# Optimization experiments

Measured on AMD Instinct MI355X. Metric: run time of the kernel, lower is better.

Reference implementation:

```python
import jax, jax.numpy as jnp
import numpy as np
from jax import lax

M = 8   # num_heads
K = 4   # num_points


def conv2d(x, w, b, pad):
    # x: [B,C,H,W], w: [O,I,kh,kw]
    y = lax.conv_general_dilated(x, w, (1, 1), [(pad, pad), (pad, pad)],
                                 dimension_numbers=('NCHW', 'OIHW', 'NCHW'))
    return y + b[None, :, None, None]


def grid_sample_zeros(v, px, py):
    # Bilinear grid_sample, align_corners=True, padding_mode='zeros'.
    # v: [N,Cm,H,W]; px,py: [N,P] in pixel coordinates.
    N, Cm, H, W = v.shape
    x0 = jnp.floor(px); y0 = jnp.floor(py)
    x1 = x0 + 1.0;      y1 = y0 + 1.0
    wx = px - x0;       wy = py - y0
    vflat = v.reshape(N, Cm, H * W)

    def tap(xi, yi):
        valid = (xi >= 0) & (xi <= W - 1) & (yi >= 0) & (yi <= H - 1)
        xc = jnp.clip(xi, 0, W - 1).astype(jnp.int32)
        yc = jnp.clip(yi, 0, H - 1).astype(jnp.int32)
        idx = yc * W + xc                          # [N,P]
        g = jnp.take_along_axis(vflat, idx[:, None, :], axis=2)  # [N,Cm,P]
        return g * valid[:, None, :].astype(v.dtype)

    v00 = tap(x0, y0); v01 = tap(x1, y0)
    v10 = tap(x0, y1); v11 = tap(x1, y1)
    wx = wx[:, None, :]; wy = wy[:, None, :]
    return (v00 * (1 - wx) * (1 - wy) + v01 * wx * (1 - wy)
            + v10 * (1 - wx) * wy + v11 * wx * wy)


def setup_inputs() -> dict:
    key = jax.random.key(0)
    ks = jax.random.split(key, 16)
    B, C, H, W = 8, 256, 64, 64
    s = 0.02
    inp = {
        'f_recalib': jax.random.normal(ks[0], (B, C, H, W), jnp.float32),
        'f_orig':    jax.random.normal(ks[1], (B, C, H, W), jnp.float32),
        'offset_w': jax.random.normal(ks[2], (M * K * 2, C, 3, 3), jnp.float32) * s,
        'offset_b': jnp.zeros((M * K * 2,), jnp.float32),
        'attn_w':   jax.random.normal(ks[3], (M * K, C, 3, 3), jnp.float32) * s,
        'attn_b':   jnp.zeros((M * K,), jnp.float32),
        'value_w':  jax.random.normal(ks[4], (C, C, 1, 1), jnp.float32) * s,
        'value_b':  jnp.zeros((C,), jnp.float32),
        'proj_w':   jax.random.normal(ks[5], (C, C, 1, 1), jnp.float32) * s,
        'proj_b':   jnp.zeros((C,), jnp.float32),
        'mlp_w1':   jax.random.normal(ks[6], (2 * C, C, 1, 1), jnp.float32) * s,
        'mlp_b1':   jnp.zeros((2 * C,), jnp.float32),
        'mlp_w2':   jax.random.normal(ks[7], (C, 2 * C, 1, 1), jnp.float32) * s,
        'mlp_b2':   jnp.zeros((C,), jnp.float32),
    }
    return inp


def reference(f_recalib, f_orig, offset_w, offset_b, attn_w, attn_b,
              value_w, value_b, proj_w, proj_b,
              mlp_w1, mlp_b1, mlp_w2, mlp_b2):
    B, C, H, W = f_recalib.shape
    Cm = C // M

    offsets = conv2d(f_recalib, offset_w, offset_b, 1).reshape(B, M, K, 2, H, W)
    attn = conv2d(f_recalib, attn_w, attn_b, 1).reshape(B, M, K, H, W)
    attn = jax.nn.softmax(attn, axis=2)
    value = conv2d(f_recalib, value_w, value_b, 0)

    gy, gx = jnp.meshgrid(jnp.arange(H, dtype=jnp.float32),
                          jnp.arange(W, dtype=jnp.float32), indexing='ij')
    gx_sym = (W - 1) - gx  # horizontally mirrored x coordinate
    # pixel-space sampling locations (align_corners=True normalization is exactly
    # inverted by grid_sample's unnormalization, so work in pixel coords)
    px = gx_sym[None, None, None] + offsets[:, :, :, 0]  # [B,M,K,H,W]
    py = gy[None, None, None] + offsets[:, :, :, 1]

    v = value.reshape(B * M, Cm, H, W)
    sampled = grid_sample_zeros(v, px.reshape(B * M, -1), py.reshape(B * M, -1))
    sampled = sampled.reshape(B, M, Cm, K, H, W)

    out = (sampled * attn[:, :, None]).sum(axis=3).reshape(B, C, H, W)
    out = conv2d(out, proj_w, proj_b, 0) + f_orig
    h = jax.nn.relu(conv2d(out, mlp_w1, mlp_b1, 0))
    out = conv2d(h, mlp_w2, mlp_b2, 0) + out
    return out
```

## Files before the change

kernel.cpp:

```cpp
#include <hip/hip_runtime.h>
#include <cstddef>

#define P_ 4096
#define PW_ 66

using u16 = unsigned short;
typedef float  f32x4  __attribute__((ext_vector_type(4)));
typedef u16    u16x8  __attribute__((ext_vector_type(8)));
typedef u16    u16x4  __attribute__((ext_vector_type(4)));
typedef __bf16 bf16x8 __attribute__((ext_vector_type(8)));

#define DEVINL __device__ __forceinline__

DEVINL u16 f2bf(float f) {
    union { float f; unsigned u; } v; v.f = f;
    unsigned r = v.u + 0x7fffu + ((v.u >> 16) & 1u);
    return (u16)(r >> 16);
}
DEVINL float bf2f(u16 h) {
    union { unsigned u; float f; } v; v.u = ((unsigned)h) << 16;
    return v.f;
}

DEVINL f32x4 mfma16(u16x8 a, u16x8 b, f32x4 c) {
    return __builtin_amdgcn_mfma_f32_16x16x32_bf16(
        __builtin_bit_cast(bf16x8, a), __builtin_bit_cast(bf16x8, b), c, 0, 0, 0);
}

DEVINL void gload16(const u16* src, const u16* lds_dst) {
    __builtin_amdgcn_global_load_lds(
        (const __attribute__((address_space(1))) void*)src,
        (__attribute__((address_space(3))) void*)lds_dst, 16, 0, 0);
}

__global__ void prep_weights(const float* __restrict__ off_w, const float* __restrict__ attn_w,
                             const float* __restrict__ val_w, const float* __restrict__ proj_w,
                             const float* __restrict__ w1, const float* __restrict__ w2,
                             u16* __restrict__ wbf) {
    int idx = blockIdx.x * 256 + threadIdx.x;
    if (idx >= 614400) return;
    float v;
    if (idx < 221184) {
        int tap = idx / 24576, rem = idx - tap * 24576, oc = rem >> 8, ic = rem & 255;
        v = (oc < 64) ? off_w[(size_t)(oc * 256 + ic) * 9 + tap]
                      : attn_w[(size_t)((oc - 64) * 256 + ic) * 9 + tap];
    } else if (idx < 286720) v = val_w[idx - 221184];
    else if (idx < 352256)   v = proj_w[idx - 286720];
    else if (idx < 483328)   v = w1[idx - 352256];
    else                     v = w2[idx - 483328];
    wbf[idx] = f2bf(v);
}

__global__ __launch_bounds__(256) void zero_pad(u16* __restrict__ xp) {
    const int b = blockIdx.x, t = threadIdx.x;
    const u16x8 z = (u16x8){0, 0, 0, 0, 0, 0, 0, 0};
    for (int q = t; q < 8320; q += 256) {
        const int p = q >> 5, chunk = q & 31;
        int row, col;
        if (p < 66)       { row = 0;  col = p; }
        else if (p < 132) { row = 65; col = p - 66; }
        else { const int q2 = p - 132; row = 1 + (q2 >> 1); col = (q2 & 1) * 65; }
        *(u16x8*)&xp[((size_t)(b * PW_ + row) * PW_ + col) * 256 + chunk * 8] = z;
    }
}

__global__ __launch_bounds__(256) void to_nhwc_pad(const float* __restrict__ in,
                                                   u16* __restrict__ xp) {
    const int y = blockIdx.x, c0 = blockIdx.y * 64, b = blockIdx.z;
    __shared__ u16 ts[64 * 72];
    const int t = threadIdx.x, cl = t >> 4, xq = t & 15;
    #pragma unroll
    for (int r = 0; r < 4; ++r) {
        const int c = r * 16 + cl;
        const float4 v = *(const float4*)&in[((size_t)(b * 256 + c0 + c)) * P_ + y * 64 + xq * 4];
        ts[(xq * 4 + 0) * 72 + c] = f2bf(v.x);
        ts[(xq * 4 + 1) * 72 + c] = f2bf(v.y);
        ts[(xq * 4 + 2) * 72 + c] = f2bf(v.z);
        ts[(xq * 4 + 3) * 72 + c] = f2bf(v.w);
    }
    __syncthreads();
    const int px = t >> 2, seg = t & 3;
    u16x8 o0, o1;
    #pragma unroll
    for (int j = 0; j < 8; ++j) {
        o0[j] = ts[px * 72 + seg * 16 + j];
        o1[j] = ts[px * 72 + seg * 16 + 8 + j];
    }
    const size_t base = ((size_t)(b * PW_ + y + 1) * PW_ + 1 + px) * 256 + c0 + seg * 16;
    *(u16x8*)&xp[base]     = o0;
    *(u16x8*)&xp[base + 8] = o1;
}

__global__ __launch_bounds__(256, 4) void conv3x3_mfma(
    const u16* __restrict__ xp, const u16* __restrict__ wconv,
    const float* __restrict__ off_b, const float* __restrict__ attn_b,
    u16* __restrict__ convout) {
    const int y = blockIdx.x, b = blockIdx.y;
    const int tid = threadIdx.x, w = tid >> 6, lane = tid & 63, g = lane >> 4, i = lane & 15;
    const int wm = w & 1, wn = w >> 1;
    const int srow = lane >> 4, sc = lane & 15;
    __shared__ u16 xs[64 * 128];
    __shared__ u16 wsL[96 * 128];

    f32x4 acc[2][3];
    #pragma unroll
    for (int mi = 0; mi < 2; ++mi)
        #pragma unroll
        for (int nj = 0; nj < 3; ++nj) acc[mi][nj] = (f32x4){0.f, 0.f, 0.f, 0.f};

    for (int tap = 0; tap < 9; ++tap) {
        const int dy = tap / 3, dx = tap % 3;
        const u16* xrow = xp + ((size_t)(b * PW_ + y + dy) * PW_ + dx) * 256;
        const u16* wt = wconv + (size_t)(tap * 96) * 256;
        for (int cc = 0; cc < 2; ++cc) {
            const int kc = cc * 128;
            #pragma unroll
            for (int t = 0; t < 4; ++t) {
                const int j = w * 4 + t;
                const int row = j * 4 + srow;
                const int cs = sc ^ (row & 7);
                gload16(xrow + (size_t)row * 256 + kc + (cs << 3), &xs[j * 512]);
            }
            #pragma unroll
            for (int t = 0; t < 6; ++t) {
                const int j = w * 6 + t;
                const int row = j * 4 + srow;
                const int cs = sc ^ (row & 7);
                gload16(wt + (size_t)row * 256 + kc + (cs << 3), &wsL[j * 512]);
            }
            __syncthreads();
            #pragma unroll
            for (int ks = 0; ks < 4; ++ks) {
                u16x8 a[2], bb[3];
                #pragma unroll
                for (int mi = 0; mi < 2; ++mi) {
                    const int pr = wm * 32 + mi * 16 + i;
                    a[mi] = *(const u16x8*)&xs[pr * 128 + (((ks * 4 + g) ^ (pr & 7)) << 3)];
                }
                #pragma unroll
                for (int nj = 0; nj < 3; ++nj) {
                    const int ocr = wn * 48 + nj * 16 + i;
                    bb[nj] = *(const u16x8*)&wsL[ocr * 128 + (((ks * 4 + g) ^ (ocr & 7)) << 3)];
                }
                #pragma unroll
                for (int mi = 0; mi < 2; ++mi)
                    #pragma unroll
                    for (int nj = 0; nj < 3; ++nj)
                        acc[mi][nj] = mfma16(a[mi], bb[nj], acc[mi][nj]);
            }
            __syncthreads();
        }
    }
    #pragma unroll
    for (int mi = 0; mi < 2; ++mi) {
        const int x0 = wm * 32 + mi * 16 + g * 4;
        #pragma unroll
        for (int nj = 0; nj < 3; ++nj) {
            const int oc = wn * 48 + nj * 16 + i;
            const float bv = (oc < 64) ? off_b[oc] : attn_b[oc - 64];
            #pragma unroll
            for (int r = 0; r < 4; ++r)
                convout[((size_t)(b * P_ + y * 64 + x0 + r)) * 96 + oc] =
                    f2bf(acc[mi][nj][r] + bv);
        }
    }
}

__global__ __launch_bounds__(256, 2) void gemm_dbuf(
    const u16* __restrict__ X, const u16* __restrict__ W,
    const float* __restrict__ bias, const void* __restrict__ resid,
    void* __restrict__ outA, u16* __restrict__ outB,
    const int KTOT, const int OC, const int mode, const int padded) {
    const int px0 = blockIdx.x * 128, oc0 = blockIdx.y * 128, b = blockIdx.z;
    const int tid = threadIdx.x, w = tid >> 6, lane = tid & 63, g = lane >> 4, i = lane & 15;
    const int wm = w & 1, wn = w >> 1;
    __shared__ u16 lds[32768];
    u16* xs = lds;
    u16* wsL = lds + 16384;

    const int srcC = (lane & 7) ^ ((lane >> 3) & 7);

    f32x4 acc[4][4];
    #pragma unroll
    for (int mi = 0; mi < 4; ++mi)
        #pragma unroll
        for (int nj = 0; nj < 4; ++nj) acc[mi][nj] = (f32x4){0.f, 0.f, 0.f, 0.f};

    const int NC = KTOT >> 6;

    auto stage = [&](int buf, int kc) {
        #pragma unroll
        for (int t = 0; t < 4; ++t) {
            const int j = w * 4 + t;
            const int row = j * 8 + (lane >> 3);
            const u16* sx;
            if (padded) {
                const int pxg = px0 + row;
                sx = X + ((size_t)(b * PW_ + (pxg >> 6) + 1) * PW_ + (pxg & 63) + 1) * 256
                       + kc + (srcC << 3);
            } else {
                sx = X + (size_t)(b * P_ + px0 + row) * KTOT + kc + (srcC << 3);
            }
            gload16(sx, &xs[buf * 8192 + j * 512]);
        }
        #pragma unroll
        for (int t = 0; t < 4; ++t) {
            const int j = w * 4 + t;
            const int row = j * 8 + (lane >> 3);
            gload16(W + (size_t)(oc0 + row) * KTOT + kc + (srcC << 3),
                    &wsL[buf * 8192 + j * 512]);
        }
    };

    stage(0, 0);
    stage(1, 64);
    asm volatile("s_waitcnt vmcnt(8)" ::: "memory");
    __builtin_amdgcn_s_barrier();

    for (int c = 0; c < NC; ++c) {
        const u16* xb = &xs[(c & 1) * 8192];
        const u16* wb = &wsL[(c & 1) * 8192];
        #pragma unroll
        for (int ks = 0; ks < 2; ++ks) {
            u16x8 a[4], bb[4];
            #pragma unroll
            for (int mi = 0; mi < 4; ++mi) {
                const int row = wm * 64 + mi * 16 + i;
                a[mi] = *(const u16x8*)&xb[row * 64 + (((ks * 4 + g) ^ (row & 7)) << 3)];
            }
            #pragma unroll
            for (int nj = 0; nj < 4; ++nj) {
                const int row = wn * 64 + nj * 16 + i;
                bb[nj] = *(const u16x8*)&wb[row * 64 + (((ks * 4 + g) ^ (row & 7)) << 3)];
            }
            #pragma unroll
            for (int mi = 0; mi < 4; ++mi)
                #pragma unroll
                for (int nj = 0; nj < 4; ++nj)
                    acc[mi][nj] = mfma16(a[mi], bb[nj], acc[mi][nj]);
        }
        __builtin_amdgcn_sched_barrier(0);
        __builtin_amdgcn_s_barrier();
        if (c + 2 < NC) {
            stage(c & 1, (c + 2) << 6);
            asm volatile("s_waitcnt vmcnt(8)" ::: "memory");
        } else {
            asm volatile("s_waitcnt vmcnt(0)" ::: "memory");
        }
        __builtin_amdgcn_s_barrier();
    }

    float* lf = (float*)lds;
    const int pxq = tid >> 2, segq = tid & 3;
    const int oclh = tid >> 1, shh = (tid & 1) * 32;

    #pragma unroll
    for (int h = 0; h < 2; ++h) {
        if (wm == h) {
            #pragma unroll
            for (int nj = 0; nj < 4; ++nj) {
                const int ocl = wn * 64 + nj * 16 + i;
                const float bv = bias[oc0 + ocl];
                #pragma unroll
                for (int mi = 0; mi < 4; ++mi)
                    #pragma unroll
                    for (int r = 0; r < 4; ++r)
                        lf[ocl * 66 + mi * 16 + g * 4 + r] = acc[mi][nj][r] + bv;
            }
        }
        __syncthreads();
        const int pxg0 = px0 + h * 64;

        if (mode == 4) {
            const float* rf = (const float*)resid;
            const size_t rb = ((size_t)b * 256 + oc0 + oclh) * P_ + pxg0 + shh;
            #pragma unroll
            for (int q = 0; q < 8; ++q) {
                const float4 r4 = *(const float4*)&rf[rb + q * 4];
                lf[oclh * 66 + shh + q * 4 + 0] += r4.x;
                lf[oclh * 66 + shh + q * 4 + 1] += r4.y;
                lf[oclh * 66 + shh + q * 4 + 2] += r4.z;
                lf[oclh * 66 + shh + q * 4 + 3] += r4.w;
            }
            __syncthreads();
        }

        if (mode <= 1 || mode == 4) {
            const size_t nb = ((size_t)(b * P_ + pxg0 + pxq)) * OC + oc0 + segq * 32;
            #pragma unroll
            for (int t2 = 0; t2 < 4; ++t2) {
                u16x8 o8;
                #pragma unroll
                for (int jj = 0; jj < 8; ++jj) {
                    float v = lf[(segq * 32 + t2 * 8 + jj) * 66 + pxq];
                    if (mode == 1) v = fmaxf(v, 0.f);
                    o8[jj] = f2bf(v);
                }
                *(u16x8*)&outB[nb + t2 * 8] = o8;
            }
        }
        if (mode == 4) {
            u16* on = (u16*)outA;
            const size_t cb = ((size_t)b * 256 + oc0 + oclh) * P_ + pxg0 + shh;
            #pragma unroll
            for (int t2 = 0; t2 < 4; ++t2) {
                u16x8 o8;
                #pragma unroll
                for (int jj = 0; jj < 8; ++jj)
                    o8[jj] = f2bf(lf[oclh * 66 + shh + t2 * 8 + jj]);
                *(u16x8*)&on[cb + t2 * 8] = o8;
            }
        }
        if (mode == 5) {
            const u16* rb16 = (const u16*)resid;
            float* of = (float*)outA;
            const size_t cb = ((size_t)b * 256 + oc0 + oclh) * P_ + pxg0 + shh;
            #pragma unroll
            for (int q = 0; q < 8; ++q) {
                const u16x4 r4 = *(const u16x4*)&rb16[cb + q * 4];
                float4 o;
                o.x = lf[oclh * 66 + shh + q * 4 + 0] + bf2f(r4[0]);
                o.y = lf[oclh * 66 + shh + q * 4 + 1] + bf2f(r4[1]);
                o.z = lf[oclh * 66 + shh + q * 4 + 2] + bf2f(r4[2]);
                o.w = lf[oclh * 66 + shh + q * 4 + 3] + bf2f(r4[3]);
                *(float4*)&of[cb + q * 4] = o;
            }
        }
        __syncthreads();
    }
}

__global__ __launch_bounds__(256) void sample_attend_bf(
    const u16* __restrict__ value, const u16* __restrict__ conv,
    u16* __restrict__ out1) {
    const int y = blockIdx.x, m = blockIdx.y, b = blockIdx.z;
    const int tid = threadIdx.x, x = tid >> 2, gq = tid & 3;
    const size_t prow = (size_t)(b * P_ + y * 64 + x);

    const u16x8 ov = *(const u16x8*)&conv[prow * 96 + m * 8];
    const u16x4 av = *(const u16x4*)&conv[prow * 96 + 64 + m * 4];

    float a[4];
    #pragma unroll
    for (int k = 0; k < 4; ++k) a[k] = bf2f(av[k]);
    const float mx = fmaxf(fmaxf(a[0], a[1]), fmaxf(a[2], a[3]));
    float s = 0.f;
    #pragma unroll
    for (int k = 0; k < 4; ++k) { a[k] = __expf(a[k] - mx); s += a[k]; }
    const float inv = 1.f / s;

    float acc[8];
    #pragma unroll
    for (int j = 0; j < 8; ++j) acc[j] = 0.f;

    const u16* vb = value + ((size_t)b * P_) * 256 + m * 32 + gq * 8;

    #pragma unroll
    for (int k = 0; k < 4; ++k) {
        const float offx = bf2f(ov[2 * k]), offy = bf2f(ov[2 * k + 1]);
        const float px = (float)(63 - x) + offx;
        const float py = (float)y + offy;
        const float x0f = floorf(px), y0f = floorf(py);
        const int xi0 = (int)x0f, yi0 = (int)y0f;
        const float wx = px - x0f, wy = py - y0f;
        const int xi1 = xi0 + 1, yi1 = yi0 + 1;
        const bool vx0 = (xi0 >= 0) & (xi0 <= 63), vx1 = (xi1 >= 0) & (xi1 <= 63);
        const bool vy0 = (yi0 >= 0) & (yi0 <= 63), vy1 = (yi1 >= 0) & (yi1 <= 63);
        const int cx0 = min(max(xi0, 0), 63), cx1 = min(max(xi1, 0), 63);
        const int cy0 = min(max(yi0, 0), 63), cy1 = min(max(yi1, 0), 63);
        const float ak = a[k] * inv;
        const float c00 = ak * (1.f - wx) * (1.f - wy) * ((vx0 & vy0) ? 1.f : 0.f);
        const float c01 = ak * wx * (1.f - wy) * ((vx1 & vy0) ? 1.f : 0.f);
        const float c10 = ak * (1.f - wx) * wy * ((vx0 & vy1) ? 1.f : 0.f);
        const float c11 = ak * wx * wy * ((vx1 & vy1) ? 1.f : 0.f);
        const u16x8 v00 = *(const u16x8*)&vb[(size_t)(cy0 * 64 + cx0) * 256];
        const u16x8 v01 = *(const u16x8*)&vb[(size_t)(cy0 * 64 + cx1) * 256];
        const u16x8 v10 = *(const u16x8*)&vb[(size_t)(cy1 * 64 + cx0) * 256];
        const u16x8 v11 = *(const u16x8*)&vb[(size_t)(cy1 * 64 + cx1) * 256];
        #pragma unroll
        for (int j = 0; j < 8; ++j)
            acc[j] += c00 * bf2f(v00[j]) + c01 * bf2f(v01[j])
                    + c10 * bf2f(v10[j]) + c11 * bf2f(v11[j]);
    }
    u16x8 o;
    #pragma unroll
    for (int j = 0; j < 8; ++j) o[j] = f2bf(acc[j]);
    *(u16x8*)&out1[prow * 256 + m * 32 + gq * 8] = o;
}

extern "C" void kernel_launch(void* const* d_in, const int* in_sizes, int n_in,
                              void* d_out, int out_size, void* d_ws, size_t ws_size,
                              hipStream_t stream) {
    const float* f_recalib = (const float*)d_in[0];
    const float* f_orig    = (const float*)d_in[1];
    const float* offset_w  = (const float*)d_in[2];
    const float* offset_b  = (const float*)d_in[3];
    const float* attn_w    = (const float*)d_in[4];
    const float* attn_b    = (const float*)d_in[5];
    const float* value_w   = (const float*)d_in[6];
    const float* value_b   = (const float*)d_in[7];
    const float* proj_w    = (const float*)d_in[8];
    const float* proj_b    = (const float*)d_in[9];
    const float* mlp_w1    = (const float*)d_in[10];
    const float* mlp_b1    = (const float*)d_in[11];
    const float* mlp_w2    = (const float*)d_in[12];
    const float* mlp_b2    = (const float*)d_in[13];
    float* out = (float*)d_out;

    u16* wsb       = (u16*)d_ws;
    u16* x_pad     = wsb;
    u16* convout   = wsb + 8921088;
    u16* value_bf  = wsb + 12066816;
    u16* out1_bf   = wsb + 20455424;
    u16* wbf       = wsb + 28844032;
    u16* out2_nchw = wsb + 29458432;
    u16* out2_bf   = x_pad;
    u16* h_bf      = wsb + 8921088;

    u16* wconv = wbf;
    u16* wval  = wbf + 221184;
    u16* wproj = wbf + 286720;
    u16* wmlp1 = wbf + 352256;
    u16* wmlp2 = wbf + 483328;

    prep_weights<<<2400, 256, 0, stream>>>(offset_w, attn_w, value_w, proj_w,
                                           mlp_w1, mlp_w2, wbf);
    zero_pad<<<8, 256, 0, stream>>>(x_pad);
    to_nhwc_pad<<<dim3(64, 4, 8), 256, 0, stream>>>(f_recalib, x_pad);
    conv3x3_mfma<<<dim3(64, 8), 256, 0, stream>>>(x_pad, wconv, offset_b, attn_b, convout);
    gemm_dbuf<<<dim3(32, 2, 8), 256, 0, stream>>>(x_pad, wval, value_b, nullptr,
                                                  nullptr, value_bf, 256, 256, 0, 1);
    sample_attend_bf<<<dim3(64, 8, 8), 256, 0, stream>>>(value_bf, convout, out1_bf);
    gemm_dbuf<<<dim3(32, 2, 8), 256, 0, stream>>>(out1_bf, wproj, proj_b, f_orig,
                                                  out2_nchw, out2_bf, 256, 256, 4, 0);
    gemm_dbuf<<<dim3(32, 4, 8), 256, 0, stream>>>(out2_bf, wmlp1, mlp_b1, nullptr,
                                                  nullptr, h_bf, 256, 512, 1, 0);
    gemm_dbuf<<<dim3(32, 2, 8), 256, 0, stream>>>(h_bf, wmlp2, mlp_b2, out2_nchw,
                                                  out, nullptr, 512, 256, 5, 0);
}
```

Before: 150.1 us.

## Stage value row window in LDS for sampling and fold pad zeroing into transpose

The sampling kernel now asynchronously loads an 8-row window of value pixels for its head into shared memory and serves bilinear taps from LDS when both taps fall inside that window, falling back to global loads otherwise. This is meant to cut repeated scattered global/L2 reads of the same value vectors. Separately, the zero_pad kernel launch is removed and border zeroing is done by the y==0 blocks of to_nhwc_pad, saving one launch. It adds 32KB LDS per block, which may reduce occupancy, and a block-wide sync.

```diff
diff --git a/kernel.cpp b/kernel.cpp
--- a/kernel.cpp
+++ b/kernel.cpp
@@ -51,24 +51,24 @@
     wbf[idx] = f2bf(v);
 }
 
-__global__ __launch_bounds__(256) void zero_pad(u16* __restrict__ xp) {
-    const int b = blockIdx.x, t = threadIdx.x;
-    const u16x8 z = (u16x8){0, 0, 0, 0, 0, 0, 0, 0};
-    for (int q = t; q < 8320; q += 256) {
-        const int p = q >> 5, chunk = q & 31;
-        int row, col;
-        if (p < 66)       { row = 0;  col = p; }
-        else if (p < 132) { row = 65; col = p - 66; }
-        else { const int q2 = p - 132; row = 1 + (q2 >> 1); col = (q2 & 1) * 65; }
-        *(u16x8*)&xp[((size_t)(b * PW_ + row) * PW_ + col) * 256 + chunk * 8] = z;
-    }
-}
-
 __global__ __launch_bounds__(256) void to_nhwc_pad(const float* __restrict__ in,
                                                    u16* __restrict__ xp) {
     const int y = blockIdx.x, c0 = blockIdx.y * 64, b = blockIdx.z;
     __shared__ u16 ts[64 * 72];
     const int t = threadIdx.x, cl = t >> 4, xq = t & 15;
+
+    if (y == 0) {
+        const u16x8 z = (u16x8){0, 0, 0, 0, 0, 0, 0, 0};
+        for (int q = t; q < 2080; q += 256) {
+            const int p = q >> 3, c8 = q & 7;
+            int row, col;
+            if (p < 66)       { row = 0;  col = p; }
+            else if (p < 132) { row = 65; col = p - 66; }
+            else { const int q2 = p - 132; row = 1 + (q2 >> 1); col = (q2 & 1) * 65; }
+            *(u16x8*)&xp[((size_t)(b * PW_ + row) * PW_ + col) * 256 + c0 + c8 * 8] = z;
+        }
+    }
+
     #pragma unroll
     for (int r = 0; r < 4; ++r) {
         const int c = r * 16 + cl;
@@ -335,11 +335,22 @@
     u16* __restrict__ out1) {
     const int y = blockIdx.x, m = blockIdx.y, b = blockIdx.z;
     const int tid = threadIdx.x, x = tid >> 2, gq = tid & 3;
+    const int w = tid >> 6, lane = tid & 63;
+    const int wlo = max(0, y - 3), whi = min(63, y + 4);
+    const int nchunks = (whi - wlo + 1) * 256;
+    __shared__ u16 vlds[8 * 64 * 32];
+
+    const u16* vbase = value + ((size_t)b * P_) * 256 + m * 32;
+    for (int it = w; it * 64 < nchunks; it += 4) {
+        const int cid = it * 64 + lane;
+        const int r = cid >> 8, px = (cid >> 2) & 63, cc = cid & 3;
+        gload16(vbase + ((size_t)((wlo + r) * 64 + px)) * 256 + cc * 8,
+                &vlds[it * 512]);
+    }
+
     const size_t prow = (size_t)(b * P_ + y * 64 + x);
-
     const u16x8 ov = *(const u16x8*)&conv[prow * 96 + m * 8];
     const u16x4 av = *(const u16x4*)&conv[prow * 96 + 64 + m * 4];
-
     float a[4];
     #pragma unroll
     for (int k = 0; k < 4; ++k) a[k] = bf2f(av[k]);
@@ -349,11 +360,11 @@
     for (int k = 0; k < 4; ++k) { a[k] = __expf(a[k] - mx); s += a[k]; }
     const float inv = 1.f / s;
 
+    __syncthreads();
+
     float acc[8];
     #pragma unroll
     for (int j = 0; j < 8; ++j) acc[j] = 0.f;
-
-    const u16* vb = value + ((size_t)b * P_) * 256 + m * 32 + gq * 8;
 
     #pragma unroll
     for (int k = 0; k < 4; ++k) {
@@ -373,10 +384,21 @@
         const float c01 = ak * wx * (1.f - wy) * ((vx1 & vy0) ? 1.f : 0.f);
         const float c10 = ak * (1.f - wx) * wy * ((vx0 & vy1) ? 1.f : 0.f);
         const float c11 = ak * wx * wy * ((vx1 & vy1) ? 1.f : 0.f);
-        const u16x8 v00 = *(const u16x8*)&vb[(size_t)(cy0 * 64 + cx0) * 256];
-        const u16x8 v01 = *(const u16x8*)&vb[(size_t)(cy0 * 64 + cx1) * 256];
-        const u16x8 v10 = *(const u16x8*)&vb[(size_t)(cy1 * 64 + cx0) * 256];
-        const u16x8 v11 = *(const u16x8*)&vb[(size_t)(cy1 * 64 + cx1) * 256];
+        u16x8 v00, v01, v10, v11;
+        const bool inWin = (cy0 >= wlo) & (cy1 <= whi);
+        if (inWin) {
+            const int r0 = (cy0 - wlo) * 64, r1 = (cy1 - wlo) * 64;
+            v00 = *(const u16x8*)&vlds[(r0 + cx0) * 32 + gq * 8];
+            v01 = *(const u16x8*)&vlds[(r0 + cx1) * 32 + gq * 8];
+            v10 = *(const u16x8*)&vlds[(r1 + cx0) * 32 + gq * 8];
+            v11 = *(const u16x8*)&vlds[(r1 + cx1) * 32 + gq * 8];
+        } else {
+            const u16* vb = vbase + gq * 8;
+            v00 = *(const u16x8*)&vb[(size_t)(cy0 * 64 + cx0) * 256];
+            v01 = *(const u16x8*)&vb[(size_t)(cy0 * 64 + cx1) * 256];
+            v10 = *(const u16x8*)&vb[(size_t)(cy1 * 64 + cx0) * 256];
+            v11 = *(const u16x8*)&vb[(size_t)(cy1 * 64 + cx1) * 256];
+        }
         #pragma unroll
         for (int j = 0; j < 8; ++j)
             acc[j] += c00 * bf2f(v00[j]) + c01 * bf2f(v01[j])
@@ -425,7 +447,6 @@
 
     prep_weights<<<2400, 256, 0, stream>>>(offset_w, attn_w, value_w, proj_w,
                                            mlp_w1, mlp_w2, wbf);
-    zero_pad<<<8, 256, 0, stream>>>(x_pad);
     to_nhwc_pad<<<dim3(64, 4, 8), 256, 0, stream>>>(f_recalib, x_pad);
     conv3x3_mfma<<<dim3(64, 8), 256, 0, stream>>>(x_pad, wconv, offset_b, attn_b, convout);
     gemm_dbuf<<<dim3(32, 2, 8), 256, 0, stream>>>(x_pad, wval, value_b, nullptr,
```

New measurement: 150.2 us. No clear change (+0.1%).
